# Performance work log

Hardware: AMD Instinct MI355X
Metric: run time of the kernel (lower is better)

The kernel has to match this reference:

```python
import jax, jax.numpy as jnp
import numpy as np

N_NODES = 10000
N_EDGES = 160000
D = 512            # input_dim = hidden_size = output_dim
NUM_EXPERTS = 4
N_LAYERS = 2


def setup_inputs() -> dict:
    key = jax.random.key(0)
    k = jax.random.split(key, 7)
    x = jax.random.normal(k[0], (N_NODES, D), dtype=jnp.float32)
    edge_index = jax.random.randint(k[1], (2, N_EDGES), 0, N_NODES, dtype=jnp.int32)
    # Gating network (Linear D -> NUM_EXPERTS)
    gate_w = jax.random.normal(k[2], (D, NUM_EXPERTS), dtype=jnp.float32) * 0.05
    gate_b = jnp.zeros((NUM_EXPERTS,), dtype=jnp.float32)
    # Per-expert SAGEConv weights: lin_r (self/root) and lin_l (neighbor) + bias
    w_self = jax.random.normal(k[3], (NUM_EXPERTS, N_LAYERS, D, D), dtype=jnp.float32) * 0.05
    w_neigh = jax.random.normal(k[4], (NUM_EXPERTS, N_LAYERS, D, D), dtype=jnp.float32) * 0.05
    b_exp = jnp.zeros((NUM_EXPERTS, N_LAYERS, D), dtype=jnp.float32)
    return {"x": x, "edge_index": edge_index, "gate_w": gate_w, "gate_b": gate_b,
            "w_self": w_self, "w_neigh": w_neigh, "b_exp": b_exp, "top_k": 1}


def reference(x, edge_index, gate_w, gate_b, w_self, w_neigh, b_exp, top_k):
    n = x.shape[0]
    src, dst = edge_index[0], edge_index[1]
    # mean-aggregation normalization (PyG SAGEConv aggr='mean'); 0 for isolated nodes
    deg = jax.ops.segment_sum(jnp.ones_like(src, dtype=x.dtype), dst, num_segments=n)
    inv_deg = jnp.where(deg > 0, 1.0 / jnp.maximum(deg, 1.0), 0.0)[:, None]  # [N,1]

    # gating: softmax(Linear(x)) then top-k routing
    gate = jax.nn.softmax(x @ gate_w + gate_b, axis=-1)          # [N, E]
    top_vals, top_idx = jax.lax.top_k(gate, top_k)               # [N, k]

    def expert(ws, wn, b):  # ws, wn: [L, D, D]; b: [L, D]
        h = x
        for l in range(N_LAYERS):
            agg = jax.ops.segment_sum(h[src], dst, num_segments=n) * inv_deg
            # SAGEConv: lin_l(mean_neigh) + lin_r(x) + bias, then relu (norm='id', eval dropout)
            h = jax.nn.relu(agg @ wn[l] + h @ ws[l] + b[l])
        return h

    # dense all-expert compute (matches original module)
    outs = jax.vmap(expert)(w_self, w_neigh, b_exp)              # [E, N, D]
    outs = jnp.transpose(outs, (1, 0, 2))                        # [N, E, D]
    sel = jnp.take_along_axis(outs, top_idx[:, :, None], axis=1)  # [N, k, D]
    return jnp.sum(sel * top_vals[:, :, None], axis=1)           # [N, D]
```

## Files before the change

kernel.cpp:

```cpp
#include <hip/hip_runtime.h>
#include <hip/hip_bf16.h>
#include <cstdint>

#define N_NODES 10000
#define N_EDGES 160000
#define DIM 512
#define K1 1024
#define NEXP 4

typedef __bf16 bf16_t;
typedef bf16_t bf16x8 __attribute__((ext_vector_type(8)));
typedef float f32x4 __attribute__((ext_vector_type(4)));

#define AS1(p) ((__attribute__((address_space(1))) void*)(p))
#define AS3(p) ((__attribute__((address_space(3))) void*)(p))

#define VMW(N) asm volatile("s_waitcnt vmcnt(" #N ")" ::: "memory")
#define MFMA16(d, a_, b_) d = __builtin_amdgcn_mfma_f32_16x16x32_bf16(a_, b_, d, 0, 0, 0)

__global__ void zero_kernel(int* __restrict__ deg, int* __restrict__ ecnt) {
    int i = blockIdx.x * blockDim.x + threadIdx.x;
    if (i < N_NODES) deg[i] = 0;
    if (i < NEXP) ecnt[i] = 0;
}

__global__ void gate_kernel(const float* __restrict__ x,
                            const float* __restrict__ gw,
                            const float* __restrict__ gb,
                            int* __restrict__ top_idx,
                            float* __restrict__ top_val,
                            bf16_t* __restrict__ acat) {
    const int wave = threadIdx.x >> 6;
    const int lane = threadIdx.x & 63;
    const int node = blockIdx.x * 4 + wave;
    if (node >= N_NODES) return;
    const float4* x4 = (const float4*)(x + (size_t)node * DIM);
    const float4* gw4 = (const float4*)gw;
    float4 xa = x4[lane * 2];
    float4 xb = x4[lane * 2 + 1];
    float xv[8] = { xa.x, xa.y, xa.z, xa.w, xb.x, xb.y, xb.z, xb.w };
    float a0 = 0.f, a1 = 0.f, a2 = 0.f, a3 = 0.f;
    #pragma unroll
    for (int c = 0; c < 8; c++) {
        float4 g = gw4[lane * 8 + c];
        a0 += xv[c] * g.x; a1 += xv[c] * g.y; a2 += xv[c] * g.z; a3 += xv[c] * g.w;
    }
    bf16x8 o;
    #pragma unroll
    for (int c = 0; c < 8; c++) o[c] = (bf16_t)xv[c];
    *(bf16x8*)(acat + (size_t)node * K1 + DIM + lane * 8) = o;
    for (int off = 32; off > 0; off >>= 1) {
        a0 += __shfl_xor(a0, off);
        a1 += __shfl_xor(a1, off);
        a2 += __shfl_xor(a2, off);
        a3 += __shfl_xor(a3, off);
    }
    if (lane == 0) {
        float z[4] = { a0 + gb[0], a1 + gb[1], a2 + gb[2], a3 + gb[3] };
        int bi = 0; float bm = z[0];
        for (int e = 1; e < 4; e++) if (z[e] > bm) { bm = z[e]; bi = e; }
        float den = 0.f;
        for (int e = 0; e < 4; e++) den += expf(z[e] - bm);
        top_idx[node] = bi;
        top_val[node] = 1.0f / den;
    }
}

__global__ void bucket_kernel(const int* __restrict__ top_idx,
                              int* __restrict__ ecnt,
                              int* __restrict__ lists) {
    __shared__ int lcnt[NEXP];
    __shared__ int base[NEXP];
    const int tid = threadIdx.x;
    if (tid < NEXP) lcnt[tid] = 0;
    __syncthreads();
    const int node = blockIdx.x * 256 + tid;
    int e = 0, rank = 0;
    if (node < N_NODES) {
        e = top_idx[node];
        rank = atomicAdd(&lcnt[e], 1);
    }
    __syncthreads();
    if (tid < NEXP) base[tid] = atomicAdd(&ecnt[tid], lcnt[tid]);
    __syncthreads();
    if (node < N_NODES) lists[e * N_NODES + base[e] + rank] = node;
}

__global__ void jobs_kernel(const int* __restrict__ ecnt, int* __restrict__ jobs) {
    if (threadIdx.x == 0 && blockIdx.x == 0) {
        int pref = 0;
        for (int e = 0; e < NEXP; e++) {
            jobs[e] = pref;
            pref += (ecnt[e] + 127) >> 7;
        }
        jobs[4] = pref;
    }
}

__global__ void deg_kernel(const int* __restrict__ dst, int* __restrict__ deg) {
    int i = blockIdx.x * blockDim.x + threadIdx.x;
    if (i < N_EDGES) atomicAdd(&deg[dst[i]], 1);
}

__global__ void scan_kernel(const int* __restrict__ deg,
                            int* __restrict__ offs,
                            int* __restrict__ cursor) {
    __shared__ int wsum[16];
    __shared__ int carrysh;
    const int tid = threadIdx.x;
    const int lane = tid & 63;
    const int wv = tid >> 6;
    if (tid == 0) carrysh = 0;
    __syncthreads();
    for (int base = 0; base < N_NODES; base += 1024) {
        int i = base + tid;
        int v = (i < N_NODES) ? deg[i] : 0;
        int s = v;
        #pragma unroll
        for (int off = 1; off < 64; off <<= 1) {
            int t = __shfl_up(s, off);
            if (lane >= off) s += t;
        }
        if (lane == 63) wsum[wv] = s;
        int carry = carrysh;
        __syncthreads();
        if (wv == 0) {
            int w = (lane < 16) ? wsum[lane] : 0;
            #pragma unroll
            for (int off = 1; off < 16; off <<= 1) {
                int t = __shfl_up(w, off);
                if (lane >= off) w += t;
            }
            if (lane < 16) wsum[lane] = w;
        }
        __syncthreads();
        int wbase = (wv > 0) ? wsum[wv - 1] : 0;
        int excl = carry + wbase + s - v;
        if (i < N_NODES) { offs[i] = excl; cursor[i] = excl; }
        int total = wsum[15];
        __syncthreads();
        if (tid == 0) carrysh = carry + total;
        __syncthreads();
    }
    if (tid == 0) offs[N_NODES] = carrysh;
}

__global__ void fill_kernel(const int* __restrict__ src, const int* __restrict__ dst,
                            int* __restrict__ cursor, int* __restrict__ csr) {
    int i = blockIdx.x * blockDim.x + threadIdx.x;
    if (i < N_EDGES) {
        int d = dst[i];
        int p = atomicAdd(&cursor[d], 1);
        csr[p] = src[i];
    }
}

__global__ void wtrans_kernel(const float* __restrict__ w_neigh,
                              const float* __restrict__ w_self,
                              bf16_t* __restrict__ Bt) {
    __shared__ float tile[32][33];
    const int m = blockIdx.z;
    const bool isSelf = m >= 8;
    const int el = m & 7;
    const float* W = (isSelf ? w_self : w_neigh) + (size_t)el * DIM * DIM;
    const int k0 = blockIdx.x * 32;
    const int n0 = blockIdx.y * 32;
    const int tx = threadIdx.x, ty = threadIdx.y;
    for (int r = ty; r < 32; r += 8)
        tile[r][tx] = W[(size_t)(k0 + r) * DIM + n0 + tx];
    __syncthreads();
    for (int r = ty; r < 32; r += 8) {
        int n = n0 + r;
        int k = k0 + tx;
        Bt[((size_t)el * DIM + n) * K1 + (isSelf ? DIM : 0) + k] = (bf16_t)tile[tx][r];
    }
}

__global__ void agg1_kernel(const int* __restrict__ offs, const int* __restrict__ csr,
                            bf16_t* __restrict__ acat) {
    const int wave = threadIdx.x >> 6;
    const int lane = threadIdx.x & 63;
    const int node = blockIdx.x * 4 + wave;
    if (node >= N_NODES) return;
    const int c0 = lane * 8;
    float s[8] = {0,0,0,0,0,0,0,0};
    int beg = offs[node];
    int end = offs[node + 1];
    int d = end - beg;
    int p = beg;
    for (; p + 8 <= end; p += 8) {
        bf16x8 v[8];
        #pragma unroll
        for (int q = 0; q < 8; q++) {
            int idx = csr[p + q];
            v[q] = *(const bf16x8*)(acat + (size_t)idx * K1 + DIM + c0);
        }
        #pragma unroll
        for (int q = 0; q < 8; q++)
            #pragma unroll
            for (int k = 0; k < 8; k++) s[k] += (float)v[q][k];
    }
    for (; p + 4 <= end; p += 4) {
        bf16x8 v[4];
        #pragma unroll
        for (int q = 0; q < 4; q++) {
            int idx = csr[p + q];
            v[q] = *(const bf16x8*)(acat + (size_t)idx * K1 + DIM + c0);
        }
        #pragma unroll
        for (int q = 0; q < 4; q++)
            #pragma unroll
            for (int k = 0; k < 8; k++) s[k] += (float)v[q][k];
    }
    for (; p < end; p++) {
        int idx = csr[p];
        bf16x8 v0 = *(const bf16x8*)(acat + (size_t)idx * K1 + DIM + c0);
        #pragma unroll
        for (int k = 0; k < 8; k++) s[k] += (float)v0[k];
    }
    float w = d > 0 ? 1.0f / (float)d : 0.0f;
    bf16x8 o;
    #pragma unroll
    for (int k = 0; k < 8; k++) o[k] = (bf16_t)(s[k] * w);
    *(bf16x8*)(acat + (size_t)node * K1 + c0) = o;
}

__global__ void agg2_kernel(const int* __restrict__ offs, const int* __restrict__ csr,
                            const int* __restrict__ top_idx,
                            const bf16_t* __restrict__ h1, bf16_t* __restrict__ acat) {
    const int wave = threadIdx.x >> 6;
    const int lane = threadIdx.x & 63;
    const int node = blockIdx.x * 4 + wave;
    if (node >= N_NODES) return;
    const int c0 = lane * 8;
    const bf16_t* hb = h1 + (size_t)top_idx[node] * N_NODES * DIM;
    float s[8] = {0,0,0,0,0,0,0,0};
    int beg = offs[node];
    int end = offs[node + 1];
    int d = end - beg;
    int p = beg;
    for (; p + 8 <= end; p += 8) {
        bf16x8 v[8];
        #pragma unroll
        for (int q = 0; q < 8; q++) {
            int idx = csr[p + q];
            v[q] = *(const bf16x8*)(hb + (size_t)idx * DIM + c0);
        }
        #pragma unroll
        for (int q = 0; q < 8; q++)
            #pragma unroll
            for (int k = 0; k < 8; k++) s[k] += (float)v[q][k];
    }
    for (; p + 4 <= end; p += 4) {
        bf16x8 v[4];
        #pragma unroll
        for (int q = 0; q < 4; q++) {
            int idx = csr[p + q];
            v[q] = *(const bf16x8*)(hb + (size_t)idx * DIM + c0);
        }
        #pragma unroll
        for (int q = 0; q < 4; q++)
            #pragma unroll
            for (int k = 0; k < 8; k++) s[k] += (float)v[q][k];
    }
    for (; p < end; p++) {
        int idx = csr[p];
        bf16x8 v0 = *(const bf16x8*)(hb + (size_t)idx * DIM + c0);
        #pragma unroll
        for (int k = 0; k < 8; k++) s[k] += (float)v0[k];
    }
    float w = d > 0 ? 1.0f / (float)d : 0.0f;
    bf16x8 o;
    #pragma unroll
    for (int k = 0; k < 8; k++) o[k] = (bf16_t)(s[k] * w);
    *(bf16x8*)(acat + (size_t)node * K1 + c0) = o;
    *(bf16x8*)(acat + (size_t)node * K1 + DIM + c0) = *(const bf16x8*)(hb + (size_t)node * DIM + c0);
}

__global__ __launch_bounds__(512, 2)
void gemm_l1_kernel(const bf16_t* __restrict__ A,
                    const bf16_t* __restrict__ Bt,
                    const float* __restrict__ bias_all,
                    bf16_t* __restrict__ h1) {
    const int b = blockIdx.x;
    const int xcd = b & 7;
    const int loc = b >> 3;
    const int mtile = xcd * 2 + (loc >> 4);
    const int ntile = loc & 15;
    const int e = ntile >> 2;

    __shared__ __align__(16) bf16_t As[3 * 640 * 32];
    __shared__ __align__(16) bf16_t Bs[3 * 128 * 32];

    const int t = threadIdx.x;
    const int lane = t & 63;
    const int wave = t >> 6;
    const int rloc = t >> 2;
    const int cgl = ((t & 3) - ((t >> 3) & 3)) & 3;

    const bf16_t* pA0 = A + (size_t)min(mtile * 640 +   0 + rloc, N_NODES - 1) * K1 + cgl * 8;
    const bf16_t* pA1 = A + (size_t)min(mtile * 640 + 128 + rloc, N_NODES - 1) * K1 + cgl * 8;
    const bf16_t* pA2 = A + (size_t)min(mtile * 640 + 256 + rloc, N_NODES - 1) * K1 + cgl * 8;
    const bf16_t* pA3 = A + (size_t)min(mtile * 640 + 384 + rloc, N_NODES - 1) * K1 + cgl * 8;
    const bf16_t* pA4 = A + (size_t)min(mtile * 640 + 512 + rloc, N_NODES - 1) * K1 + cgl * 8;
    const bf16_t* pB0 = Bt + ((size_t)(e * 2 + 0) * DIM + (ntile & 3) * 128 + rloc) * K1 + cgl * 8;

    char* asb = (char*)&As[0];
    char* bsb = (char*)&Bs[0];

    auto stage_full = [&](int bu) {
        char* ab = asb + bu * 40960 + wave * 1024;
        char* bb = bsb + bu * 8192  + wave * 1024;
        __builtin_amdgcn_global_load_lds(AS1(pA0), AS3(ab),          16, 0, 0);
        __builtin_amdgcn_global_load_lds(AS1(pA1), AS3(ab + 8192),   16, 0, 0);
        __builtin_amdgcn_global_load_lds(AS1(pA2), AS3(ab + 16384),  16, 0, 0);
        __builtin_amdgcn_global_load_lds(AS1(pA3), AS3(ab + 24576),  16, 0, 0);
        __builtin_amdgcn_global_load_lds(AS1(pA4), AS3(ab + 32768),  16, 0, 0);
        __builtin_amdgcn_global_load_lds(AS1(pB0), AS3(bb),          16, 0, 0);
        pA0 += 32; pA1 += 32; pA2 += 32; pA3 += 32; pA4 += 32; pB0 += 32;
    };

    const int rfr = lane & 15;
    const int cpr = lane >> 4;
    const int wm = wave >> 1;
    const int wn = wave & 1;
    const int arow = wm * 160 + rfr;
    const int brow = wn * 64 + rfr;
    const int ppA = (cpr + (arow >> 1)) & 3;
    const int ppB = (cpr + (brow >> 1)) & 3;
    const int aoff = arow * 32 + ppA * 8;
    const int boff = brow * 32 + ppB * 8;

    f32x4 acc[10][4] = {};

    auto compute_full = [&](int bu) {
        const bf16_t* Ab = As + bu * 20480 + aoff;
        const bf16_t* Bb = Bs + bu * 4096  + boff;
        bf16x8 bfr[4];
        #pragma unroll
        for (int j = 0; j < 4; j++) bfr[j] = *(const bf16x8*)(Bb + j * 512);
        #pragma unroll
        for (int i = 0; i < 10; i++) {
            bf16x8 af = *(const bf16x8*)(Ab + i * 512);
            #pragma unroll
            for (int j = 0; j < 4; j++)
                MFMA16(acc[i][j], af, bfr[j]);
        }
    };

    stage_full(0);
    stage_full(1);

    int cb = 0, sb = 2;
    for (int tt = 0; tt < 31; ++tt) {
        VMW(6);
        __builtin_amdgcn_s_barrier();
        asm volatile("" ::: "memory");
        const bool st = (tt < 30);
        char* ab = asb + sb * 40960 + wave * 1024;
        char* bb = bsb + sb * 8192  + wave * 1024;
        const bf16_t* Ab = As + cb * 20480 + aoff;
        const bf16_t* Bb = Bs + cb * 4096  + boff;

        bf16x8 bq[4], aq[4];

        #pragma unroll
        for (int j = 0; j < 4; j++) bq[j] = *(const bf16x8*)(Bb + j * 512);
        #pragma unroll
        for (int i = 0; i < 4; i++) aq[i] = *(const bf16x8*)(Ab + i * 512);
        if (st) {
            __builtin_amdgcn_global_load_lds(AS1(pA0), AS3(ab),        16, 0, 0);
            __builtin_amdgcn_global_load_lds(AS1(pA1), AS3(ab + 8192), 16, 0, 0);
        }
        __builtin_amdgcn_s_barrier();
        asm volatile("s_waitcnt lgkmcnt(0)" ::: "memory");
        __builtin_amdgcn_sched_barrier(0);
        __builtin_amdgcn_s_setprio(1);
        #pragma unroll
        for (int i = 0; i < 4; i++)
            #pragma unroll
            for (int j = 0; j < 4; j++)
                MFMA16(acc[i][j], aq[i], bq[j]);
        __builtin_amdgcn_s_setprio(0);
        __builtin_amdgcn_s_barrier();

        #pragma unroll
        for (int i = 0; i < 3; i++) aq[i] = *(const bf16x8*)(Ab + (4 + i) * 512);
        if (st) {
            __builtin_amdgcn_global_load_lds(AS1(pA2), AS3(ab + 16384), 16, 0, 0);
            __builtin_amdgcn_global_load_lds(AS1(pA3), AS3(ab + 24576), 16, 0, 0);
        }
        __builtin_amdgcn_s_barrier();
        asm volatile("s_waitcnt lgkmcnt(0)" ::: "memory");
        __builtin_amdgcn_sched_barrier(0);
        __builtin_amdgcn_s_setprio(1);
        #pragma unroll
        for (int i = 0; i < 3; i++)
            #pragma unroll
            for (int j = 0; j < 4; j++)
                MFMA16(acc[4 + i][j], aq[i], bq[j]);
        __builtin_amdgcn_s_setprio(0);
        __builtin_amdgcn_s_barrier();

        #pragma unroll
        for (int i = 0; i < 3; i++) aq[i] = *(const bf16x8*)(Ab + (7 + i) * 512);
        if (st) {
            __builtin_amdgcn_global_load_lds(AS1(pA4), AS3(ab + 32768), 16, 0, 0);
            __builtin_amdgcn_global_load_lds(AS1(pB0), AS3(bb),         16, 0, 0);
        }
        __builtin_amdgcn_s_barrier();
        asm volatile("s_waitcnt lgkmcnt(0)" ::: "memory");
        __builtin_amdgcn_sched_barrier(0);
        __builtin_amdgcn_s_setprio(1);
        #pragma unroll
        for (int i = 0; i < 3; i++)
            #pragma unroll
            for (int j = 0; j < 4; j++)
                MFMA16(acc[7 + i][j], aq[i], bq[j]);
        __builtin_amdgcn_s_setprio(0);
        __builtin_amdgcn_s_barrier();

        if (st) {
            pA0 += 32; pA1 += 32; pA2 += 32; pA3 += 32; pA4 += 32; pB0 += 32;
            sb = (sb == 2) ? 0 : sb + 1;
        }
        cb = (cb == 2) ? 0 : cb + 1;
    }
    VMW(0);
    __builtin_amdgcn_s_barrier();
    asm volatile("" ::: "memory");
    compute_full(cb);

    const float* bias = bias_all + e * 1024;
    const int cobase = (ntile & 3) * 128 + wn * 64 + (lane & 15);
    float bv[4];
    #pragma unroll
    for (int j = 0; j < 4; j++) bv[j] = bias[cobase + j * 16];
    const int rbase = mtile * 640 + wm * 160 + (lane >> 4) * 4;
    #pragma unroll
    for (int i = 0; i < 10; i++) {
        #pragma unroll
        for (int r = 0; r < 4; r++) {
            int row = rbase + i * 16 + r;
            if (row < N_NODES) {
                bf16_t* cp = h1 + ((size_t)e * N_NODES + row) * DIM + cobase;
                #pragma unroll
                for (int j = 0; j < 4; j++) {
                    float v = fmaxf(acc[i][j][r] + bv[j], 0.f);
                    cp[j * 16] = (bf16_t)v;
                }
            }
        }
    }
}

__global__ __launch_bounds__(256)
void gemm2_kernel(const bf16_t* __restrict__ A,
                  const bf16_t* __restrict__ Bt,
                  const float* __restrict__ bias_all,
                  float* __restrict__ out,
                  const int* __restrict__ lists,
                  const int* __restrict__ ecnt,
                  const int* __restrict__ jobs,
                  const float* __restrict__ top_val) {
    __shared__ __align__(16) bf16_t As[128 * 32];
    __shared__ __align__(16) bf16_t Bs[128 * 32];

    const int t = threadIdx.x;
    const int lane = t & 63;
    const int wave = t >> 6;
    const int wm = wave >> 1;
    const int wn = wave & 1;
    const int r0 = t >> 2;
    const int rot = (t >> 3) & 3;
    const int cgl = ((t & 3) - rot) & 3;
    const int cpr = lane >> 4;
    const int rfr = lane & 15;
    char* asb = (char*)&As[0];
    char* bsb = (char*)&Bs[0];
    const int wb = wave * 1024;

    const int total = jobs[4] * 4;

    for (int j = blockIdx.x; j < total; j += gridDim.x) {
        const int byt = j >> 2;
        const int bx = j & 3;
        const int e = (byt >= jobs[1]) + (byt >= jobs[2]) + (byt >= jobs[3]);
        const int by = byt - jobs[e];
        const int cnt = ecnt[e];

        int i0 = by * 128 + r0;
        int i1 = i0 + 64;
        int arow0 = lists[e * N_NODES + min(i0, cnt - 1)];
        int arow1 = lists[e * N_NODES + min(i1, cnt - 1)];
        const bf16_t* Bte = Bt + (size_t)(e * 2 + 1) * DIM * K1;
        const bf16_t* aptr0 = A + (size_t)arow0 * K1 + cgl * 8;
        const bf16_t* aptr1 = A + (size_t)arow1 * K1 + cgl * 8;
        const bf16_t* bptr0 = Bte + (size_t)(bx * 128 + r0) * K1 + cgl * 8;
        const bf16_t* bptr1 = bptr0 + (size_t)64 * K1;

        f32x4 acc[4][4] = {};

        for (int k0 = 0; k0 < K1; k0 += 32) {
            __syncthreads();
            __builtin_amdgcn_global_load_lds(AS1(aptr0), AS3(asb + wb),        16, 0, 0);
            __builtin_amdgcn_global_load_lds(AS1(aptr1), AS3(asb + 4096 + wb), 16, 0, 0);
            __builtin_amdgcn_global_load_lds(AS1(bptr0), AS3(bsb + wb),        16, 0, 0);
            __builtin_amdgcn_global_load_lds(AS1(bptr1), AS3(bsb + 4096 + wb), 16, 0, 0);
            __syncthreads();
            bf16x8 af[4], bfr[4];
            #pragma unroll
            for (int i = 0; i < 4; i++) {
                int r_full = wm * 64 + i * 16 + rfr;
                int p = (cpr + (r_full >> 1)) & 3;
                af[i] = *(const bf16x8*)(As + r_full * 32 + p * 8);
            }
            #pragma unroll
            for (int jj = 0; jj < 4; jj++) {
                int r_full = wn * 64 + jj * 16 + rfr;
                int p = (cpr + (r_full >> 1)) & 3;
                bfr[jj] = *(const bf16x8*)(Bs + r_full * 32 + p * 8);
            }
            #pragma unroll
            for (int i = 0; i < 4; i++)
                #pragma unroll
                for (int jj = 0; jj < 4; jj++)
                    acc[i][jj] = __builtin_amdgcn_mfma_f32_16x16x32_bf16(af[i], bfr[jj], acc[i][jj], 0, 0, 0);
            aptr0 += 32; aptr1 += 32; bptr0 += 32; bptr1 += 32;
        }

        const float* bias = bias_all + e * 1024 + DIM;
        const int cbase = bx * 128 + wn * 64 + (lane & 15);
        float bv[4];
        #pragma unroll
        for (int jj = 0; jj < 4; jj++) bv[jj] = bias[cbase + jj * 16];
        #pragma unroll
        for (int i = 0; i < 4; i++) {
            #pragma unroll
            for (int r = 0; r < 4; r++) {
                int row = by * 128 + wm * 64 + i * 16 + (lane >> 4) * 4 + r;
                if (row < cnt) {
                    int node = lists[e * N_NODES + row];
                    float tv = top_val[node];
                    float* cp = out + (size_t)node * DIM + cbase;
                    #pragma unroll
                    for (int jj = 0; jj < 4; jj++) {
                        float v = fmaxf(acc[i][jj][r] + bv[jj], 0.f);
                        cp[jj * 16] = v * tv;
                    }
                }
            }
        }
    }
}

extern "C" void kernel_launch(void* const* d_in, const int* in_sizes, int n_in,
                              void* d_out, int out_size, void* d_ws, size_t ws_size,
                              hipStream_t stream) {
    const float* x       = (const float*)d_in[0];
    const int*   edge    = (const int*)d_in[1];
    const float* gw      = (const float*)d_in[2];
    const float* gb      = (const float*)d_in[3];
    const float* w_self  = (const float*)d_in[4];
    const float* w_neigh = (const float*)d_in[5];
    const float* b_exp   = (const float*)d_in[6];
    float* out = (float*)d_out;

    char* p = (char*)d_ws;
    auto alloc = [&](size_t bytes) {
        char* r = p;
        p += (bytes + 255) & ~(size_t)255;
        return r;
    };
    bf16_t* Bt      = (bf16_t*)alloc((size_t)8 * DIM * K1 * 2);
    bf16_t* acat    = (bf16_t*)alloc((size_t)N_NODES * K1 * 2);
    bf16_t* h1      = (bf16_t*)alloc((size_t)NEXP * N_NODES * DIM * 2);
    int*    deg     = (int*)alloc((size_t)N_NODES * 4);
    int*    offs    = (int*)alloc((size_t)(N_NODES + 1) * 4);
    int*    cursor  = (int*)alloc((size_t)N_NODES * 4);
    int*    csr     = (int*)alloc((size_t)N_EDGES * 4);
    int*    top_idx = (int*)alloc((size_t)N_NODES * 4);
    float*  top_val = (float*)alloc((size_t)N_NODES * 4);
    int*    ecnt    = (int*)alloc(256);
    int*    lists   = (int*)alloc((size_t)NEXP * N_NODES * 4);
    int*    jobs    = ecnt + 8;

    const int* srcE = edge;
    const int* dstE = edge + N_EDGES;

    zero_kernel<<<40, 256, 0, stream>>>(deg, ecnt);
    gate_kernel<<<N_NODES / 4, 256, 0, stream>>>(x, gw, gb, top_idx, top_val, acat);
    bucket_kernel<<<40, 256, 0, stream>>>(top_idx, ecnt, lists);
    jobs_kernel<<<1, 1, 0, stream>>>(ecnt, jobs);
    deg_kernel<<<N_EDGES / 256, 256, 0, stream>>>(dstE, deg);
    scan_kernel<<<1, 1024, 0, stream>>>(deg, offs, cursor);
    fill_kernel<<<N_EDGES / 256, 256, 0, stream>>>(srcE, dstE, cursor, csr);
    wtrans_kernel<<<dim3(16, 16, 16), dim3(32, 8), 0, stream>>>(w_neigh, w_self, Bt);
    agg1_kernel<<<N_NODES / 4, 256, 0, stream>>>(offs, csr, acat);
    gemm_l1_kernel<<<256, 512, 0, stream>>>(acat, Bt, b_exp, h1);
    agg2_kernel<<<N_NODES / 4, 256, 0, stream>>>(offs, csr, top_idx, h1, acat);
    gemm2_kernel<<<320, 256, 0, stream>>>(acat, Bt, b_exp, out, lists, ecnt, jobs, top_val);
}
```

Before: 267.9 us.

## Triple-buffer LDS tiles in gemm2 to overlap global loads with MFMA

The gemm2 K-loop changes from a single LDS buffer with two barriers per step to a three-stage ring. Direct global-to-LDS loads for upcoming K-tiles are issued ahead, and partial vmcnt waits let them overlap with MFMA compute on the current tile. The goal is to hide global memory latency and halve the barrier count. In exchange, LDS use triples, which may limit occupancy. Row indices are also clamped defensively.

```diff
diff --git a/kernel.cpp b/kernel.cpp
--- a/kernel.cpp
+++ b/kernel.cpp
@@ -463,8 +463,8 @@
                   const int* __restrict__ ecnt,
                   const int* __restrict__ jobs,
                   const float* __restrict__ top_val) {
-    __shared__ __align__(16) bf16_t As[128 * 32];
-    __shared__ __align__(16) bf16_t Bs[128 * 32];
+    __shared__ __align__(16) bf16_t As[3 * 128 * 32];
+    __shared__ __align__(16) bf16_t Bs[3 * 128 * 32];
 
     const int t = threadIdx.x;
     const int lane = t & 63;
@@ -488,11 +488,14 @@
         const int e = (byt >= jobs[1]) + (byt >= jobs[2]) + (byt >= jobs[3]);
         const int by = byt - jobs[e];
         const int cnt = ecnt[e];
+        const int cmax = max(cnt, 1);
 
         int i0 = by * 128 + r0;
         int i1 = i0 + 64;
-        int arow0 = lists[e * N_NODES + min(i0, cnt - 1)];
-        int arow1 = lists[e * N_NODES + min(i1, cnt - 1)];
+        int arow0 = lists[e * N_NODES + min(i0, cmax - 1)];
+        int arow1 = lists[e * N_NODES + min(i1, cmax - 1)];
+        arow0 = min(max(arow0, 0), N_NODES - 1);
+        arow1 = min(max(arow1, 0), N_NODES - 1);
         const bf16_t* Bte = Bt + (size_t)(e * 2 + 1) * DIM * K1;
         const bf16_t* aptr0 = A + (size_t)arow0 * K1 + cgl * 8;
         const bf16_t* aptr1 = A + (size_t)arow1 * K1 + cgl * 8;
@@ -501,33 +504,60 @@
 
         f32x4 acc[4][4] = {};
 
-        for (int k0 = 0; k0 < K1; k0 += 32) {
-            __syncthreads();
-            __builtin_amdgcn_global_load_lds(AS1(aptr0), AS3(asb + wb),        16, 0, 0);
-            __builtin_amdgcn_global_load_lds(AS1(aptr1), AS3(asb + 4096 + wb), 16, 0, 0);
-            __builtin_amdgcn_global_load_lds(AS1(bptr0), AS3(bsb + wb),        16, 0, 0);
-            __builtin_amdgcn_global_load_lds(AS1(bptr1), AS3(bsb + 4096 + wb), 16, 0, 0);
-            __syncthreads();
+        auto stage = [&](int bu) {
+            char* ab = asb + bu * 8192 + wb;
+            char* bb = bsb + bu * 8192 + wb;
+            __builtin_amdgcn_global_load_lds(AS1(aptr0), AS3(ab),        16, 0, 0);
+            __builtin_amdgcn_global_load_lds(AS1(aptr1), AS3(ab + 4096), 16, 0, 0);
+            __builtin_amdgcn_global_load_lds(AS1(bptr0), AS3(bb),        16, 0, 0);
+            __builtin_amdgcn_global_load_lds(AS1(bptr1), AS3(bb + 4096), 16, 0, 0);
+            aptr0 += 32; aptr1 += 32; bptr0 += 32; bptr1 += 32;
+        };
+
+        auto compute = [&](int bu) {
+            const bf16_t* Ab = As + bu * 4096;
+            const bf16_t* Bb = Bs + bu * 4096;
             bf16x8 af[4], bfr[4];
             #pragma unroll
             for (int i = 0; i < 4; i++) {
                 int r_full = wm * 64 + i * 16 + rfr;
                 int p = (cpr + (r_full >> 1)) & 3;
-                af[i] = *(const bf16x8*)(As + r_full * 32 + p * 8);
+                af[i] = *(const bf16x8*)(Ab + r_full * 32 + p * 8);
             }
             #pragma unroll
             for (int jj = 0; jj < 4; jj++) {
                 int r_full = wn * 64 + jj * 16 + rfr;
                 int p = (cpr + (r_full >> 1)) & 3;
-                bfr[jj] = *(const bf16x8*)(Bs + r_full * 32 + p * 8);
+                bfr[jj] = *(const bf16x8*)(Bb + r_full * 32 + p * 8);
             }
             #pragma unroll
             for (int i = 0; i < 4; i++)
                 #pragma unroll
                 for (int jj = 0; jj < 4; jj++)
-                    acc[i][jj] = __builtin_amdgcn_mfma_f32_16x16x32_bf16(af[i], bfr[jj], acc[i][jj], 0, 0, 0);
-            aptr0 += 32; aptr1 += 32; bptr0 += 32; bptr1 += 32;
-        }
+                    MFMA16(acc[i][jj], af[i], bfr[jj]);
+        };
+
+        __builtin_amdgcn_s_barrier();
+        asm volatile("" ::: "memory");
+
+        stage(0);
+        stage(1);
+        int cb = 0, sb = 2;
+        for (int tt = 0; tt < 31; ++tt) {
+            VMW(4);
+            __builtin_amdgcn_s_barrier();
+            asm volatile("" ::: "memory");
+            if (tt < 30) {
+                stage(sb);
+                sb = (sb == 2) ? 0 : sb + 1;
+            }
+            compute(cb);
+            cb = (cb == 2) ? 0 : cb + 1;
+        }
+        VMW(0);
+        __builtin_amdgcn_s_barrier();
+        asm volatile("" ::: "memory");
+        compute(cb);
 
         const float* bias = bias_all + e * 1024 + DIM;
         const int cbase = bx * 128 + wn * 64 + (lane & 15);
```

New measurement: 273.6 us. 1.02x slower.
